# Performance work log

Measured on AMD Instinct MI355X. Metric: run time of the kernel, lower is better.

## Reference

```python
import jax, jax.numpy as jnp
import numpy as np

NUM_HEADS = 8
NUM_GROUPS = 32
EMB = 512
EPS = 1e-5


def setup_inputs() -> dict:
    key = jax.random.key(0)
    ks = jax.random.split(key, 12)
    B, C, H, W = 256, EMB, 16, 16
    s = 1.0 / np.sqrt(C)
    x = jax.random.normal(ks[0], (B, C, H, W), dtype=jnp.float32)
    Wq = jax.random.normal(ks[1], (C, EMB), dtype=jnp.float32) * s
    bq = jax.random.normal(ks[2], (EMB,), dtype=jnp.float32) * 0.01
    Wk = jax.random.normal(ks[3], (C, EMB), dtype=jnp.float32) * s
    bk = jax.random.normal(ks[4], (EMB,), dtype=jnp.float32) * 0.01
    Wv = jax.random.normal(ks[5], (C, EMB), dtype=jnp.float32) * s
    bv = jax.random.normal(ks[6], (EMB,), dtype=jnp.float32) * 0.01
    Wf = jax.random.normal(ks[7], (EMB, EMB), dtype=jnp.float32) * s
    bf = jax.random.normal(ks[8], (EMB,), dtype=jnp.float32) * 0.01
    gn_w = jnp.ones((EMB,), dtype=jnp.float32)
    gn_b = jnp.zeros((EMB,), dtype=jnp.float32)
    return {"x": x, "Wq": Wq, "bq": bq, "Wk": Wk, "bk": bk,
            "Wv": Wv, "bv": bv, "Wf": Wf, "bf": bf,
            "gn_w": gn_w, "gn_b": gn_b}


def reference(x, Wq, bq, Wk, bk, Wv, bv, Wf, bf, gn_w, gn_b):
    B, C, H, W = x.shape
    S = H * W
    nh = NUM_HEADS
    dh = EMB // nh
    xs = x.reshape(B, C, S).transpose(0, 2, 1)  # [B, S, C]
    q = (xs @ Wq + bq).reshape(B, S, nh, dh)
    k = (xs @ Wk + bk).reshape(B, S, nh, dh)
    v = (xs @ Wv + bv).reshape(B, S, nh, dh)
    scale = dh ** -0.5
    logits = jnp.einsum('bshd,bthd->bhst', q, k) * scale  # [B, nh, S, S]
    attn = jax.nn.softmax(logits, axis=-1)
    o = jnp.einsum('bhst,bthd->bshd', attn, v).reshape(B, S, EMB)
    o = o @ Wf + bf  # [B, S, EMB]
    y = o.transpose(0, 2, 1).reshape(B, EMB, H, W) + x  # residual
    # GroupNorm over (channels-within-group, H, W)
    G = NUM_GROUPS
    yg = y.reshape(B, G, EMB // G, H, W)
    mu = jnp.mean(yg, axis=(2, 3, 4), keepdims=True)
    var = jnp.var(yg, axis=(2, 3, 4), keepdims=True)
    yn = ((yg - mu) * jax.lax.rsqrt(var + EPS)).reshape(B, EMB, H, W)
    return yn * gn_w.reshape(1, EMB, 1, 1) + gn_b.reshape(1, EMB, 1, 1)
```

## Files before the change

### kernel.cpp

```cpp
#include <hip/hip_runtime.h>
#include <hip/hip_bf16.h>
#include <stdint.h>

#define B_  256
#define C_  512
#define S_  256
#define NH  8
#define DH  64

typedef float f32x4 __attribute__((ext_vector_type(4)));
typedef short s16x8 __attribute__((ext_vector_type(8)));

static __device__ __forceinline__ unsigned short f2bf(float f) {
  union { float f; unsigned u; } v; v.f = f;
  unsigned r = v.u + 0x7FFFu + ((v.u >> 16) & 1u);
  return (unsigned short)(r >> 16);
}

static __device__ __forceinline__ unsigned pk_bf16(float lo, float hi) {
  unsigned r;
  asm("v_cvt_pk_bf16_f32 %0, %1, %2" : "=v"(r) : "v"(lo), "v"(hi));
  return r;
}

static __device__ __forceinline__ void gload_lds16(const void* g, void* l) {
  __builtin_amdgcn_global_load_lds((const __attribute__((address_space(1))) void*)g,
                                   (__attribute__((address_space(3))) void*)l,
                                   16, 0, 0);
}

__global__ __launch_bounds__(256) void prep(const float* __restrict__ x,
                                            const float* __restrict__ Wq,
                                            const float* __restrict__ Wk,
                                            const float* __restrict__ Wv,
                                            const float* __restrict__ Wf,
                                            unsigned short* __restrict__ Whead,
                                            unsigned short* __restrict__ Wft,
                                            unsigned short* __restrict__ xs) {
  __shared__ float tile[64][65];
  int bid = blockIdx.x;
  int t = threadIdx.x;
  int tr = t >> 4;
  int tc = (t & 15) * 4;
  if (bid < 8192) {
    int b = bid >> 5, rem = bid & 31;
    int s0 = (rem & 3) * 64, c0 = (rem >> 2) * 64;
    const float* xb = x + (size_t)b * C_ * S_;
#pragma unroll
    for (int i = 0; i < 4; ++i) {
      int c = tr + i * 16;
      float4 v = *(const float4*)&xb[(size_t)(c0 + c) * S_ + s0 + tc];
      tile[c][tc + 0] = v.x; tile[c][tc + 1] = v.y;
      tile[c][tc + 2] = v.z; tile[c][tc + 3] = v.w;
    }
    __syncthreads();
    unsigned short* xsb = xs + (size_t)b * S_ * C_;
#pragma unroll
    for (int i = 0; i < 4; ++i) {
      int s = tr + i * 16;
      ushort4 o;
      o.x = f2bf(tile[tc + 0][s]); o.y = f2bf(tile[tc + 1][s]);
      o.z = f2bf(tile[tc + 2][s]); o.w = f2bf(tile[tc + 3][s]);
      *(ushort4*)&xsb[(size_t)(s0 + s) * C_ + c0 + tc] = o;
    }
  } else {
    int r = bid - 8192;
    int mat = r >> 6, r6 = r & 63;
    int n0 = (r6 & 7) * 64, c0 = (r6 >> 3) * 64;
    const float* src = (mat == 0) ? Wq : (mat == 1) ? Wk : (mat == 2) ? Wv : Wf;
#pragma unroll
    for (int i = 0; i < 4; ++i) {
      int c = tr + i * 16;
      float4 v = *(const float4*)&src[(size_t)(c0 + c) * 512 + n0 + tc];
      tile[c][tc + 0] = v.x; tile[c][tc + 1] = v.y;
      tile[c][tc + 2] = v.z; tile[c][tc + 3] = v.w;
    }
    __syncthreads();
    int h = n0 >> 6;
    unsigned short* dst = (mat < 3) ? (Whead + ((size_t)h * 192 + mat * 64) * 512)
                                    : (Wft + (size_t)n0 * 512);
#pragma unroll
    for (int i = 0; i < 4; ++i) {
      int nl = tr + i * 16;
      ushort4 o;
      o.x = f2bf(tile[tc + 0][nl]); o.y = f2bf(tile[tc + 1][nl]);
      o.z = f2bf(tile[tc + 2][nl]); o.w = f2bf(tile[tc + 3][nl]);
      *(ushort4*)&dst[(size_t)nl * 512 + c0 + tc] = o;
    }
  }
}

#define QKP 68
#define QOFF 0
#define KOFF 34816
#define VOFF 69632
__global__ __launch_bounds__(512) void qkvattn(const unsigned short* __restrict__ xs,
                                               const unsigned short* __restrict__ Whead,
                                               const float* __restrict__ bq,
                                               const float* __restrict__ bk,
                                               const float* __restrict__ bv,
                                               unsigned short* __restrict__ o) {
  __shared__ __align__(16) char lds[114688];
  int bid = blockIdx.x;
  int lin = (bid & 7) * 256 + (bid >> 3);
  int h = lin & 7, b = lin >> 3;
  int t = threadIdx.x, lane = t & 63, w = t >> 6;
  int l15 = lane & 15, l4 = lane >> 4;
  int wr = w >> 2, wc = w & 3;
  const unsigned short* xsb = xs + (size_t)b * S_ * C_;
  const unsigned short* wh  = Whead + (size_t)h * 192 * C_;

#define FSTAGE(kt, p)                                                         \
  {                                                                           \
    _Pragma("unroll")                                                         \
    for (int i = 0; i < 4; ++i) {                                             \
      int ch = i * 512 + t, r = ch >> 3, g = ch & 7;                          \
      int gs = g ^ (r & 7);                                                   \
      gload_lds16(xsb + (size_t)r * C_ + (kt) * 64 + gs * 8,                  \
                  lds + (p) * 57344 + ch * 16);                               \
    }                                                                         \
    _Pragma("unroll")                                                         \
    for (int i = 0; i < 3; ++i) {                                             \
      int ch = i * 512 + t, r = ch >> 3, g = ch & 7;                          \
      int gs = g ^ (r & 7);                                                   \
      gload_lds16(wh + (size_t)r * C_ + (kt) * 64 + gs * 8,                   \
                  lds + (p) * 57344 + 32768 + ch * 16);                       \
    }                                                                         \
  }

  f32x4 acc[8][3] = {};
  FSTAGE(0, 0);

  for (int kt = 0; kt < 8; ++kt) {
    if (kt < 7) FSTAGE(kt + 1, (kt + 1) & 1);
    if (kt < 7) asm volatile("s_waitcnt vmcnt(7)" ::: "memory");
    else        asm volatile("s_waitcnt vmcnt(0)" ::: "memory");
    __builtin_amdgcn_s_barrier();
    asm volatile("" ::: "memory");
    const char* Ab = lds + (kt & 1) * 57344;
    const char* Bb = Ab + 32768;
#pragma unroll
    for (int kk = 0; kk < 2; ++kk) {
      s16x8 afr[8], bfr[3];
#pragma unroll
      for (int fi = 0; fi < 8; ++fi) {
        int r = wr * 128 + fi * 16 + l15;
        afr[fi] = *(const s16x8*)(Ab + r * 128 + (((kk * 4 + l4) ^ (r & 7)) << 4));
      }
#pragma unroll
      for (int fj = 0; fj < 3; ++fj) {
        int r = wc * 48 + fj * 16 + l15;
        bfr[fj] = *(const s16x8*)(Bb + r * 128 + (((kk * 4 + l4) ^ (r & 7)) << 4));
      }
      __builtin_amdgcn_s_setprio(1);
#pragma unroll
      for (int fi = 0; fi < 8; ++fi)
#pragma unroll
        for (int fj = 0; fj < 3; ++fj)
          acc[fi][fj] = __builtin_amdgcn_mfma_f32_16x16x32_bf16(afr[fi], bfr[fj], acc[fi][fj], 0, 0, 0);
      __builtin_amdgcn_s_setprio(0);
    }
    __builtin_amdgcn_s_barrier();
  }
#undef FSTAGE

  unsigned short* Ql = (unsigned short*)(lds + QOFF);
  unsigned short* Kl = (unsigned short*)(lds + KOFF);
  unsigned short* Vl = (unsigned short*)(lds + VOFF);
  int h64 = h * 64;
#pragma unroll
  for (int fj = 0; fj < 3; ++fj) {
    int n = wc * 48 + fj * 16 + l15;
    int sel = n >> 6, d = n & 63;
    const float* bias = (sel == 0) ? bq : (sel == 1) ? bk : bv;
    float bias_v = bias[h64 + d];
    if (sel == 2) {
#pragma unroll
      for (int fi = 0; fi < 8; ++fi) {
        int s0 = wr * 128 + fi * 16 + l4 * 4;
        ushort4 o4;
        o4.x = f2bf(acc[fi][fj][0] + bias_v);
        o4.y = f2bf(acc[fi][fj][1] + bias_v);
        o4.z = f2bf(acc[fi][fj][2] + bias_v);
        o4.w = f2bf(acc[fi][fj][3] + bias_v);
        *(ushort4*)&Vl[d * 264 + s0] = o4;
      }
    } else {
      unsigned short* dstl = (sel == 0) ? Ql : Kl;
#pragma unroll
      for (int fi = 0; fi < 8; ++fi)
#pragma unroll
        for (int rg = 0; rg < 4; ++rg) {
          int s = wr * 128 + fi * 16 + l4 * 4 + rg;
          int row = s;
          if (sel == 1) {
            int s64 = s & 63, w32 = s64 & 31;
            row = (s & 192) + (s64 >> 5) * 32 + ((w32 >> 2) & 1) * 16 + (w32 >> 3) * 4 + (w32 & 3);
          }
          dstl[row * QKP + d] = f2bf(acc[fi][fj][rg] + bias_v);
        }
    }
  }
  __syncthreads();

  s16x8 qf[2][2];
#pragma unroll
  for (int fi = 0; fi < 2; ++fi)
#pragma unroll
    for (int kk = 0; kk < 2; ++kk) {
      int row = w * 32 + fi * 16 + l15;
      qf[fi][kk] = *(const s16x8*)((const char*)lds + QOFF + row * (QKP * 2) + kk * 64 + l4 * 16);
    }

  f32x4 acco[4][2] = {};
  float m_run[2] = {-3e38f, -3e38f}, l_run[2] = {0.f, 0.f};
  const float SCL = 0.125f * 1.44269504089f;

  for (int kb = 0; kb < 4; ++kb) {
    f32x4 accs[4][2] = {};
#pragma unroll
    for (int kk = 0; kk < 2; ++kk) {
      s16x8 kf[4];
#pragma unroll
      for (int fj = 0; fj < 4; ++fj)
        kf[fj] = *(const s16x8*)((const char*)lds + KOFF + (kb * 64 + fj * 16 + l15) * (QKP * 2) + kk * 64 + l4 * 16);
      __builtin_amdgcn_s_setprio(1);
#pragma unroll
      for (int fj = 0; fj < 4; ++fj)
#pragma unroll
        for (int fi = 0; fi < 2; ++fi)
          accs[fj][fi] = __builtin_amdgcn_mfma_f32_16x16x32_bf16(kf[fj], qf[fi][kk], accs[fj][fi], 0, 0, 0);
      __builtin_amdgcn_s_setprio(0);
    }
#pragma unroll
    for (int fi = 0; fi < 2; ++fi) {
      float m0[4];
#pragma unroll
      for (int fj = 0; fj < 4; ++fj)
        m0[fj] = fmaxf(fmaxf(accs[fj][fi][0], accs[fj][fi][1]),
                       fmaxf(accs[fj][fi][2], accs[fj][fi][3]));
      float mx = fmaxf(fmaxf(m0[0], m0[1]), fmaxf(m0[2], m0[3]));
      mx = fmaxf(mx, __shfl_xor(mx, 16, 64));
      mx = fmaxf(mx, __shfl_xor(mx, 32, 64));
      float mnew = fmaxf(m_run[fi], mx);
      float alpha = __builtin_amdgcn_exp2f((m_run[fi] - mnew) * SCL);
      m_run[fi] = mnew;
      float s0[4];
#pragma unroll
      for (int fj = 0; fj < 4; ++fj) {
#pragma unroll
        for (int rg = 0; rg < 4; ++rg) {
          float p = __builtin_amdgcn_exp2f((accs[fj][fi][rg] - mnew) * SCL);
          accs[fj][fi][rg] = p;
        }
        s0[fj] = (accs[fj][fi][0] + accs[fj][fi][1]) + (accs[fj][fi][2] + accs[fj][fi][3]);
      }
      float lsum = (s0[0] + s0[1]) + (s0[2] + s0[3]);
      lsum += __shfl_xor(lsum, 16, 64);
      lsum += __shfl_xor(lsum, 32, 64);
      l_run[fi] = l_run[fi] * alpha + lsum;
#pragma unroll
      for (int fd = 0; fd < 4; ++fd)
#pragma unroll
        for (int rg = 0; rg < 4; ++rg) acco[fd][fi][rg] *= alpha;
    }
#pragma unroll
    for (int kk2 = 0; kk2 < 2; ++kk2) {
      s16x8 vf[4];
#pragma unroll
      for (int fd = 0; fd < 4; ++fd)
        vf[fd] = *(const s16x8*)((const char*)lds + VOFF + (fd * 16 + l15) * 528 + kb * 128 + kk2 * 64 + l4 * 16);
#pragma unroll
      for (int fi = 0; fi < 2; ++fi) {
        union { unsigned u[4]; s16x8 v; } pb;
        pb.u[0] = pk_bf16(accs[2 * kk2][fi][0],     accs[2 * kk2][fi][1]);
        pb.u[1] = pk_bf16(accs[2 * kk2][fi][2],     accs[2 * kk2][fi][3]);
        pb.u[2] = pk_bf16(accs[2 * kk2 + 1][fi][0], accs[2 * kk2 + 1][fi][1]);
        pb.u[3] = pk_bf16(accs[2 * kk2 + 1][fi][2], accs[2 * kk2 + 1][fi][3]);
        __builtin_amdgcn_s_setprio(1);
#pragma unroll
        for (int fd = 0; fd < 4; ++fd)
          acco[fd][fi] = __builtin_amdgcn_mfma_f32_16x16x32_bf16(vf[fd], pb.v, acco[fd][fi], 0, 0, 0);
        __builtin_amdgcn_s_setprio(0);
      }
    }
  }

  unsigned short* ob = o + (size_t)b * S_ * C_ + h * DH;
#pragma unroll
  for (int fi = 0; fi < 2; ++fi) {
    float inv = 1.0f / l_run[fi];
    int qrow = w * 32 + fi * 16 + l15;
#pragma unroll
    for (int fd = 0; fd < 4; ++fd) {
      ushort4 s4;
      s4.x = f2bf(acco[fd][fi][0] * inv);
      s4.y = f2bf(acco[fd][fi][1] * inv);
      s4.z = f2bf(acco[fd][fi][2] * inv);
      s4.w = f2bf(acco[fd][fi][3] * inv);
      *(ushort4*)&ob[(size_t)qrow * C_ + fd * 16 + l4 * 4] = s4;
    }
  }
}

__global__ __launch_bounds__(512, 4) void proj_gn(const unsigned short* __restrict__ o,
                                                  const unsigned short* __restrict__ Wft,
                                                  const float* __restrict__ bfp,
                                                  const float* __restrict__ x,
                                                  const float* __restrict__ gnw,
                                                  const float* __restrict__ gnb,
                                                  float* __restrict__ out) {
  __shared__ __align__(16) char plds[40960];
  __shared__ float red_s[64], red_q[64];
  __shared__ float mu_s[4], rs_s[4];
  int bid = blockIdx.x;
  int lin = (bid & 7) * 256 + (bid >> 3);
  int b = lin >> 3, ct = lin & 7;
  int t = threadIdx.x, lane = t & 63, w = t >> 6;
  int l15 = lane & 15, l4 = lane >> 4;
  if (t < 64) { red_s[t] = 0.f; red_q[t] = 0.f; }
  f32x4 acc[4][2] = {};
  const unsigned short* wt = Wft + (size_t)ct * 64 * C_;
  const unsigned short* ob = o + (size_t)b * S_ * C_;

#define PSTAGE(kt, p)                                                         \
  {                                                                           \
    if (t < 256) {                                                            \
      int r = t >> 2, g = t & 3;                                              \
      int gs = g ^ ((r >> 1) & 3);                                            \
      gload_lds16(wt + (size_t)r * C_ + (kt) * 32 + gs * 8,                   \
                  plds + (p) * 20480 + t * 16);                               \
    }                                                                         \
    _Pragma("unroll")                                                         \
    for (int i = 0; i < 2; ++i) {                                             \
      int ch = i * 512 + t, r = ch >> 2, g = ch & 3;                          \
      int gs = g ^ ((r >> 1) & 3);                                            \
      gload_lds16(ob + (size_t)r * C_ + (kt) * 32 + gs * 8,                   \
                  plds + (p) * 20480 + 4096 + ch * 16);                       \
    }                                                                         \
  }

  PSTAGE(0, 0);

  for (int kt = 0; kt < 16; ++kt) {
    if (kt < 15) {
      PSTAGE(kt + 1, (kt + 1) & 1);
      if (t < 256) asm volatile("s_waitcnt vmcnt(3)" ::: "memory");
      else         asm volatile("s_waitcnt vmcnt(2)" ::: "memory");
    } else {
      asm volatile("s_waitcnt vmcnt(0)" ::: "memory");
    }
    __builtin_amdgcn_s_barrier();
    asm volatile("" ::: "memory");
    const char* Ab = plds + (kt & 1) * 20480;
    const char* Bb = Ab + 4096;
    s16x8 af[4], bfr[2];
#pragma unroll
    for (int fi = 0; fi < 4; ++fi) {
      int r = fi * 16 + l15;
      af[fi] = *(const s16x8*)(Ab + r * 64 + ((l4 ^ ((r >> 1) & 3)) << 4));
    }
#pragma unroll
    for (int fj = 0; fj < 2; ++fj) {
      int r = w * 32 + fj * 16 + l15;
      bfr[fj] = *(const s16x8*)(Bb + r * 64 + ((l4 ^ ((r >> 1) & 3)) << 4));
    }
    __builtin_amdgcn_s_setprio(1);
#pragma unroll
    for (int fi = 0; fi < 4; ++fi)
#pragma unroll
      for (int fj = 0; fj < 2; ++fj)
        acc[fi][fj] = __builtin_amdgcn_mfma_f32_16x16x32_bf16(af[fi], bfr[fj], acc[fi][fj], 0, 0, 0);
    __builtin_amdgcn_s_setprio(0);
    __builtin_amdgcn_s_barrier();
  }
#undef PSTAGE

  const float* xb = x + (size_t)b * C_ * S_;
  int c_base = ct * 64;
  int s_base = w * 32;
#pragma unroll
  for (int fi = 0; fi < 4; ++fi)
#pragma unroll
    for (int rg = 0; rg < 4; ++rg) {
      int cl = fi * 16 + l4 * 4 + rg;
      int c = c_base + cl;
      float bias_v = bfp[c];
      float psum = 0.f, psq = 0.f;
#pragma unroll
      for (int fj = 0; fj < 2; ++fj) {
        int s = s_base + fj * 16 + l15;
        float y = acc[fi][fj][rg] + bias_v + xb[(size_t)c * S_ + s];
        acc[fi][fj][rg] = y;
        psum += y; psq += y * y;
      }
#pragma unroll
      for (int off = 1; off < 16; off <<= 1) {
        psum += __shfl_xor(psum, off, 64);
        psq += __shfl_xor(psq, off, 64);
      }
      if (l15 == 0) {
        atomicAdd(&red_s[cl], psum);
        atomicAdd(&red_q[cl], psq);
      }
    }
  __syncthreads();
  if (t < 4) {
    float s = 0.f, qq = 0.f;
#pragma unroll
    for (int i = 0; i < 16; ++i) { s += red_s[t * 16 + i]; qq += red_q[t * 16 + i]; }
    float mu = s * (1.0f / 4096.0f);
    float var = qq * (1.0f / 4096.0f) - mu * mu;
    mu_s[t] = mu;
    rs_s[t] = rsqrtf(var + 1e-5f);
  }
  __syncthreads();
  float* outb = out + (size_t)b * C_ * S_;
#pragma unroll
  for (int fi = 0; fi < 4; ++fi)
#pragma unroll
    for (int rg = 0; rg < 4; ++rg) {
      int cl = fi * 16 + l4 * 4 + rg;
      int c = c_base + cl;
      int gl = cl >> 4;
      float mu = mu_s[gl], rs = rs_s[gl];
      float gw = gnw[c], gb = gnb[c];
#pragma unroll
      for (int fj = 0; fj < 2; ++fj) {
        int s = s_base + fj * 16 + l15;
        outb[(size_t)c * S_ + s] = (acc[fi][fj][rg] - mu) * rs * gw + gb;
      }
    }
}

extern "C" void kernel_launch(void* const* d_in, const int* in_sizes, int n_in,
                              void* d_out, int out_size, void* d_ws, size_t ws_size,
                              hipStream_t stream) {
  const float* x   = (const float*)d_in[0];
  const float* Wq  = (const float*)d_in[1];
  const float* bq  = (const float*)d_in[2];
  const float* Wk  = (const float*)d_in[3];
  const float* bk  = (const float*)d_in[4];
  const float* Wv  = (const float*)d_in[5];
  const float* bv  = (const float*)d_in[6];
  const float* Wf  = (const float*)d_in[7];
  const float* bf  = (const float*)d_in[8];
  const float* gnw = (const float*)d_in[9];
  const float* gnb = (const float*)d_in[10];

  char* ws = (char*)d_ws;
  unsigned short* Whead = (unsigned short*)ws;
  unsigned short* Wft   = (unsigned short*)(ws + 0x180000);
  unsigned short* xs    = (unsigned short*)(ws + 0x200000);
  unsigned short* obuf  = (unsigned short*)(ws + 0x200000 + (size_t)B_ * S_ * C_ * 2);
  float* out = (float*)d_out;

  hipLaunchKernelGGL(prep, dim3(8448), dim3(256), 0, stream,
                     x, Wq, Wk, Wv, Wf, Whead, Wft, xs);
  hipLaunchKernelGGL(qkvattn, dim3(2048), dim3(512), 0, stream,
                     xs, Whead, bq, bk, bv, obuf);
  hipLaunchKernelGGL(proj_gn, dim3(2048), dim3(512), 0, stream,
                     obuf, Wft, bf, x, gnw, gnb, out);
}
```

Baseline: 314.7 us.

## Transpose QKV projection MFMA tiling to vectorize Q/K LDS stores

Swaps the operand roles in the fused QKV projection so weight rows feed the A slot and x rows feed the B slot. The per-wave tile changes from 8x3 to 6x4 fragments, which puts four consecutive head dims in each lane. This lets the Q/K epilogue pack two bf16 pairs into one 8-byte LDS store and load the bias as a float4. V is now written with scalar stores and a new row stride of 266 elements to reduce bank conflicts. That stride leaves the 16-byte V fragment reads in the attention loop misaligned, which may split into narrower loads or be unsafe.

```diff
diff --git a/kernel.cpp b/kernel.cpp
--- a/kernel.cpp
+++ b/kernel.cpp
@@ -94,6 +94,7 @@
 #define QOFF 0
 #define KOFF 34816
 #define VOFF 69632
+#define VSTR 266
 __global__ __launch_bounds__(512) void qkvattn(const unsigned short* __restrict__ xs,
                                                const unsigned short* __restrict__ Whead,
                                                const float* __restrict__ bq,
@@ -128,7 +129,7 @@
     }                                                                         \
   }
 
-  f32x4 acc[8][3] = {};
+  f32x4 acc[6][4] = {};
   FSTAGE(0, 0);
 
   for (int kt = 0; kt < 8; ++kt) {
@@ -141,23 +142,23 @@
     const char* Bb = Ab + 32768;
 #pragma unroll
     for (int kk = 0; kk < 2; ++kk) {
-      s16x8 afr[8], bfr[3];
-#pragma unroll
-      for (int fi = 0; fi < 8; ++fi) {
-        int r = wr * 128 + fi * 16 + l15;
-        afr[fi] = *(const s16x8*)(Ab + r * 128 + (((kk * 4 + l4) ^ (r & 7)) << 4));
-      }
-#pragma unroll
-      for (int fj = 0; fj < 3; ++fj) {
-        int r = wc * 48 + fj * 16 + l15;
-        bfr[fj] = *(const s16x8*)(Bb + r * 128 + (((kk * 4 + l4) ^ (r & 7)) << 4));
+      s16x8 wfr[6], xfr[4];
+#pragma unroll
+      for (int fi = 0; fi < 6; ++fi) {
+        int r = wr * 96 + fi * 16 + l15;
+        wfr[fi] = *(const s16x8*)(Bb + r * 128 + (((kk * 4 + l4) ^ (r & 7)) << 4));
+      }
+#pragma unroll
+      for (int fj = 0; fj < 4; ++fj) {
+        int r = wc * 64 + fj * 16 + l15;
+        xfr[fj] = *(const s16x8*)(Ab + r * 128 + (((kk * 4 + l4) ^ (r & 7)) << 4));
       }
       __builtin_amdgcn_s_setprio(1);
 #pragma unroll
-      for (int fi = 0; fi < 8; ++fi)
-#pragma unroll
-        for (int fj = 0; fj < 3; ++fj)
-          acc[fi][fj] = __builtin_amdgcn_mfma_f32_16x16x32_bf16(afr[fi], bfr[fj], acc[fi][fj], 0, 0, 0);
+      for (int fi = 0; fi < 6; ++fi)
+#pragma unroll
+        for (int fj = 0; fj < 4; ++fj)
+          acc[fi][fj] = __builtin_amdgcn_mfma_f32_16x16x32_bf16(wfr[fi], xfr[fj], acc[fi][fj], 0, 0, 0);
       __builtin_amdgcn_s_setprio(0);
     }
     __builtin_amdgcn_s_barrier();
@@ -169,36 +170,36 @@
   unsigned short* Vl = (unsigned short*)(lds + VOFF);
   int h64 = h * 64;
 #pragma unroll
-  for (int fj = 0; fj < 3; ++fj) {
-    int n = wc * 48 + fj * 16 + l15;
-    int sel = n >> 6, d = n & 63;
+  for (int fi = 0; fi < 6; ++fi) {
+    int n0q = wr * 96 + fi * 16 + l4 * 4;
+    int sel = n0q >> 6;
+    int d0 = n0q & 63;
     const float* bias = (sel == 0) ? bq : (sel == 1) ? bk : bv;
-    float bias_v = bias[h64 + d];
+    float4 b4 = *(const float4*)&bias[h64 + d0];
     if (sel == 2) {
 #pragma unroll
-      for (int fi = 0; fi < 8; ++fi) {
-        int s0 = wr * 128 + fi * 16 + l4 * 4;
-        ushort4 o4;
-        o4.x = f2bf(acc[fi][fj][0] + bias_v);
-        o4.y = f2bf(acc[fi][fj][1] + bias_v);
-        o4.z = f2bf(acc[fi][fj][2] + bias_v);
-        o4.w = f2bf(acc[fi][fj][3] + bias_v);
-        *(ushort4*)&Vl[d * 264 + s0] = o4;
+      for (int fj = 0; fj < 4; ++fj) {
+        int s = wc * 64 + fj * 16 + l15;
+        Vl[(d0 + 0) * VSTR + s] = f2bf(acc[fi][fj][0] + b4.x);
+        Vl[(d0 + 1) * VSTR + s] = f2bf(acc[fi][fj][1] + b4.y);
+        Vl[(d0 + 2) * VSTR + s] = f2bf(acc[fi][fj][2] + b4.z);
+        Vl[(d0 + 3) * VSTR + s] = f2bf(acc[fi][fj][3] + b4.w);
       }
     } else {
       unsigned short* dstl = (sel == 0) ? Ql : Kl;
 #pragma unroll
-      for (int fi = 0; fi < 8; ++fi)
-#pragma unroll
-        for (int rg = 0; rg < 4; ++rg) {
-          int s = wr * 128 + fi * 16 + l4 * 4 + rg;
-          int row = s;
-          if (sel == 1) {
-            int s64 = s & 63, w32 = s64 & 31;
-            row = (s & 192) + (s64 >> 5) * 32 + ((w32 >> 2) & 1) * 16 + (w32 >> 3) * 4 + (w32 & 3);
-          }
-          dstl[row * QKP + d] = f2bf(acc[fi][fj][rg] + bias_v);
+      for (int fj = 0; fj < 4; ++fj) {
+        int s = wc * 64 + fj * 16 + l15;
+        int row = s;
+        if (sel == 1) {
+          int s64 = s & 63, w32 = s64 & 31;
+          row = (s & 192) + (s64 >> 5) * 32 + ((w32 >> 2) & 1) * 16 + (w32 >> 3) * 4 + (w32 & 3);
         }
+        unsigned u0 = pk_bf16(acc[fi][fj][0] + b4.x, acc[fi][fj][1] + b4.y);
+        unsigned u1 = pk_bf16(acc[fi][fj][2] + b4.z, acc[fi][fj][3] + b4.w);
+        uint2 val; val.x = u0; val.y = u1;
+        *(uint2*)&dstl[row * QKP + d0] = val;
+      }
     }
   }
   __syncthreads();
@@ -269,7 +270,7 @@
       s16x8 vf[4];
 #pragma unroll
       for (int fd = 0; fd < 4; ++fd)
-        vf[fd] = *(const s16x8*)((const char*)lds + VOFF + (fd * 16 + l15) * 528 + kb * 128 + kk2 * 64 + l4 * 16);
+        vf[fd] = *(const s16x8*)((const char*)lds + VOFF + (fd * 16 + l15) * (VSTR * 2) + kb * 128 + kk2 * 64 + l4 * 16);
 #pragma unroll
       for (int fi = 0; fi < 2; ++fi) {
         union { unsigned u[4]; s16x8 v; } pb;
```

Result: no change. 315.0 us (+0.1%).

## Double qkvattn block to 1024 threads, halving per-wave tiles

Applied to the files above, without the earlier changes.

The fused QKV-projection and attention kernel now runs 16 waves per block instead of 8. Each wave owns a 64x48 projection tile and 16 query rows instead of 128x48 and 32 rows. The staging loads are redistributed over 1024 threads, with per-thread vmcnt waits adjusted to match. The aim is more latency hiding per CU with fewer accumulator registers per wave. The cost is less reuse of fragments loaded from LDS and more barrier participants, and LDS use (about 112KB per block) still limits the CU to one block.

```diff
diff --git a/kernel.cpp b/kernel.cpp
--- a/kernel.cpp
+++ b/kernel.cpp
@@ -94,12 +94,12 @@
 #define QOFF 0
 #define KOFF 34816
 #define VOFF 69632
-__global__ __launch_bounds__(512) void qkvattn(const unsigned short* __restrict__ xs,
-                                               const unsigned short* __restrict__ Whead,
-                                               const float* __restrict__ bq,
-                                               const float* __restrict__ bk,
-                                               const float* __restrict__ bv,
-                                               unsigned short* __restrict__ o) {
+__global__ __launch_bounds__(1024, 4) void qkvattn(const unsigned short* __restrict__ xs,
+                                                   const unsigned short* __restrict__ Whead,
+                                                   const float* __restrict__ bq,
+                                                   const float* __restrict__ bk,
+                                                   const float* __restrict__ bv,
+                                                   unsigned short* __restrict__ o) {
   __shared__ __align__(16) char lds[114688];
   int bid = blockIdx.x;
   int lin = (bid & 7) * 256 + (bid >> 3);
@@ -113,38 +113,47 @@
 #define FSTAGE(kt, p)                                                         \
   {                                                                           \
     _Pragma("unroll")                                                         \
-    for (int i = 0; i < 4; ++i) {                                             \
-      int ch = i * 512 + t, r = ch >> 3, g = ch & 7;                          \
+    for (int i = 0; i < 2; ++i) {                                             \
+      int ch = i * 1024 + t, r = ch >> 3, g = ch & 7;                         \
       int gs = g ^ (r & 7);                                                   \
       gload_lds16(xsb + (size_t)r * C_ + (kt) * 64 + gs * 8,                  \
                   lds + (p) * 57344 + ch * 16);                               \
     }                                                                         \
-    _Pragma("unroll")                                                         \
-    for (int i = 0; i < 3; ++i) {                                             \
-      int ch = i * 512 + t, r = ch >> 3, g = ch & 7;                          \
+    {                                                                         \
+      int ch = t, r = ch >> 3, g = ch & 7;                                    \
       int gs = g ^ (r & 7);                                                   \
       gload_lds16(wh + (size_t)r * C_ + (kt) * 64 + gs * 8,                   \
                   lds + (p) * 57344 + 32768 + ch * 16);                       \
     }                                                                         \
-  }
-
-  f32x4 acc[8][3] = {};
+    if (t < 512) {                                                            \
+      int ch = 1024 + t, r = ch >> 3, g = ch & 7;                             \
+      int gs = g ^ (r & 7);                                                   \
+      gload_lds16(wh + (size_t)r * C_ + (kt) * 64 + gs * 8,                   \
+                  lds + (p) * 57344 + 32768 + ch * 16);                       \
+    }                                                                         \
+  }
+
+  f32x4 acc[4][3] = {};
   FSTAGE(0, 0);
 
   for (int kt = 0; kt < 8; ++kt) {
-    if (kt < 7) FSTAGE(kt + 1, (kt + 1) & 1);
-    if (kt < 7) asm volatile("s_waitcnt vmcnt(7)" ::: "memory");
-    else        asm volatile("s_waitcnt vmcnt(0)" ::: "memory");
+    if (kt < 7) {
+      FSTAGE(kt + 1, (kt + 1) & 1);
+      if (t < 512) asm volatile("s_waitcnt vmcnt(4)" ::: "memory");
+      else         asm volatile("s_waitcnt vmcnt(3)" ::: "memory");
+    } else {
+      asm volatile("s_waitcnt vmcnt(0)" ::: "memory");
+    }
     __builtin_amdgcn_s_barrier();
     asm volatile("" ::: "memory");
     const char* Ab = lds + (kt & 1) * 57344;
     const char* Bb = Ab + 32768;
 #pragma unroll
     for (int kk = 0; kk < 2; ++kk) {
-      s16x8 afr[8], bfr[3];
-#pragma unroll
-      for (int fi = 0; fi < 8; ++fi) {
-        int r = wr * 128 + fi * 16 + l15;
+      s16x8 afr[4], bfr[3];
+#pragma unroll
+      for (int fi = 0; fi < 4; ++fi) {
+        int r = wr * 64 + fi * 16 + l15;
         afr[fi] = *(const s16x8*)(Ab + r * 128 + (((kk * 4 + l4) ^ (r & 7)) << 4));
       }
 #pragma unroll
@@ -154,7 +163,7 @@
       }
       __builtin_amdgcn_s_setprio(1);
 #pragma unroll
-      for (int fi = 0; fi < 8; ++fi)
+      for (int fi = 0; fi < 4; ++fi)
 #pragma unroll
         for (int fj = 0; fj < 3; ++fj)
           acc[fi][fj] = __builtin_amdgcn_mfma_f32_16x16x32_bf16(afr[fi], bfr[fj], acc[fi][fj], 0, 0, 0);
@@ -176,8 +185,8 @@
     float bias_v = bias[h64 + d];
     if (sel == 2) {
 #pragma unroll
-      for (int fi = 0; fi < 8; ++fi) {
-        int s0 = wr * 128 + fi * 16 + l4 * 4;
+      for (int fi = 0; fi < 4; ++fi) {
+        int s0 = wr * 64 + fi * 16 + l4 * 4;
         ushort4 o4;
         o4.x = f2bf(acc[fi][fj][0] + bias_v);
         o4.y = f2bf(acc[fi][fj][1] + bias_v);
@@ -188,10 +197,10 @@
     } else {
       unsigned short* dstl = (sel == 0) ? Ql : Kl;
 #pragma unroll
-      for (int fi = 0; fi < 8; ++fi)
+      for (int fi = 0; fi < 4; ++fi)
 #pragma unroll
         for (int rg = 0; rg < 4; ++rg) {
-          int s = wr * 128 + fi * 16 + l4 * 4 + rg;
+          int s = wr * 64 + fi * 16 + l4 * 4 + rg;
           int row = s;
           if (sel == 1) {
             int s64 = s & 63, w32 = s64 & 31;
@@ -203,21 +212,19 @@
   }
   __syncthreads();
 
-  s16x8 qf[2][2];
-#pragma unroll
-  for (int fi = 0; fi < 2; ++fi)
-#pragma unroll
-    for (int kk = 0; kk < 2; ++kk) {
-      int row = w * 32 + fi * 16 + l15;
-      qf[fi][kk] = *(const s16x8*)((const char*)lds + QOFF + row * (QKP * 2) + kk * 64 + l4 * 16);
-    }
-
-  f32x4 acco[4][2] = {};
-  float m_run[2] = {-3e38f, -3e38f}, l_run[2] = {0.f, 0.f};
+  s16x8 qf[2];
+#pragma unroll
+  for (int kk = 0; kk < 2; ++kk) {
+    int row = w * 16 + l15;
+    qf[kk] = *(const s16x8*)((const char*)lds + QOFF + row * (QKP * 2) + kk * 64 + l4 * 16);
+  }
+
+  f32x4 acco[4] = {};
+  float m_run = -3e38f, l_run = 0.f;
   const float SCL = 0.125f * 1.44269504089f;
 
   for (int kb = 0; kb < 4; ++kb) {
-    f32x4 accs[4][2] = {};
+    f32x4 accs[4] = {};
 #pragma unroll
     for (int kk = 0; kk < 2; ++kk) {
       s16x8 kf[4];
@@ -227,42 +234,38 @@
       __builtin_amdgcn_s_setprio(1);
 #pragma unroll
       for (int fj = 0; fj < 4; ++fj)
-#pragma unroll
-        for (int fi = 0; fi < 2; ++fi)
-          accs[fj][fi] = __builtin_amdgcn_mfma_f32_16x16x32_bf16(kf[fj], qf[fi][kk], accs[fj][fi], 0, 0, 0);
+        accs[fj] = __builtin_amdgcn_mfma_f32_16x16x32_bf16(kf[fj], qf[kk], accs[fj], 0, 0, 0);
       __builtin_amdgcn_s_setprio(0);
     }
-#pragma unroll
-    for (int fi = 0; fi < 2; ++fi) {
+    {
       float m0[4];
 #pragma unroll
       for (int fj = 0; fj < 4; ++fj)
-        m0[fj] = fmaxf(fmaxf(accs[fj][fi][0], accs[fj][fi][1]),
-                       fmaxf(accs[fj][fi][2], accs[fj][fi][3]));
+        m0[fj] = fmaxf(fmaxf(accs[fj][0], accs[fj][1]), fmaxf(accs[fj][2], accs[fj][3]));
       float mx = fmaxf(fmaxf(m0[0], m0[1]), fmaxf(m0[2], m0[3]));
       mx = fmaxf(mx, __shfl_xor(mx, 16, 64));
       mx = fmaxf(mx, __shfl_xor(mx, 32, 64));
-      float mnew = fmaxf(m_run[fi], mx);
-      float alpha = __builtin_amdgcn_exp2f((m_run[fi] - mnew) * SCL);
-      m_run[fi] = mnew;
+      float mnew = fmaxf(m_run, mx);
+      float alpha = __builtin_amdgcn_exp2f((m_run - mnew) * SCL);
+      m_run = mnew;
       float s0[4];
 #pragma unroll
       for (int fj = 0; fj < 4; ++fj) {
 #pragma unroll
         for (int rg = 0; rg < 4; ++rg) {
-          float p = __builtin_amdgcn_exp2f((accs[fj][fi][rg] - mnew) * SCL);
-          accs[fj][fi][rg] = p;
+          float p = __builtin_amdgcn_exp2f((accs[fj][rg] - mnew) * SCL);
+          accs[fj][rg] = p;
         }
-        s0[fj] = (accs[fj][fi][0] + accs[fj][fi][1]) + (accs[fj][fi][2] + accs[fj][fi][3]);
+        s0[fj] = (accs[fj][0] + accs[fj][1]) + (accs[fj][2] + accs[fj][3]);
       }
       float lsum = (s0[0] + s0[1]) + (s0[2] + s0[3]);
       lsum += __shfl_xor(lsum, 16, 64);
       lsum += __shfl_xor(lsum, 32, 64);
-      l_run[fi] = l_run[fi] * alpha + lsum;
+      l_run = l_run * alpha + lsum;
 #pragma unroll
       for (int fd = 0; fd < 4; ++fd)
 #pragma unroll
-        for (int rg = 0; rg < 4; ++rg) acco[fd][fi][rg] *= alpha;
+        for (int rg = 0; rg < 4; ++rg) acco[fd][rg] *= alpha;
     }
 #pragma unroll
     for (int kk2 = 0; kk2 < 2; ++kk2) {
@@ -270,34 +273,30 @@
 #pragma unroll
       for (int fd = 0; fd < 4; ++fd)
         vf[fd] = *(const s16x8*)((const char*)lds + VOFF + (fd * 16 + l15) * 528 + kb * 128 + kk2 * 64 + l4 * 16);
-#pragma unroll
-      for (int fi = 0; fi < 2; ++fi) {
-        union { unsigned u[4]; s16x8 v; } pb;
-        pb.u[0] = pk_bf16(accs[2 * kk2][fi][0],     accs[2 * kk2][fi][1]);
-        pb.u[1] = pk_bf16(accs[2 * kk2][fi][2],     accs[2 * kk2][fi][3]);
-        pb.u[2] = pk_bf16(accs[2 * kk2 + 1][fi][0], accs[2 * kk2 + 1][fi][1]);
-        pb.u[3] = pk_bf16(accs[2 * kk2 + 1][fi][2], accs[2 * kk2 + 1][fi][3]);
-        __builtin_amdgcn_s_setprio(1);
-#pragma unroll
-        for (int fd = 0; fd < 4; ++fd)
-          acco[fd][fi] = __builtin_amdgcn_mfma_f32_16x16x32_bf16(vf[fd], pb.v, acco[fd][fi], 0, 0, 0);
-        __builtin_amdgcn_s_setprio(0);
-      }
+      union { unsigned u[4]; s16x8 v; } pb;
+      pb.u[0] = pk_bf16(accs[2 * kk2][0],     accs[2 * kk2][1]);
+      pb.u[1] = pk_bf16(accs[2 * kk2][2],     accs[2 * kk2][3]);
+      pb.u[2] = pk_bf16(accs[2 * kk2 + 1][0], accs[2 * kk2 + 1][1]);
+      pb.u[3] = pk_bf16(accs[2 * kk2 + 1][2], accs[2 * kk2 + 1][3]);
+      __builtin_amdgcn_s_setprio(1);
+#pragma unroll
+      for (int fd = 0; fd < 4; ++fd)
+        acco[fd] = __builtin_amdgcn_mfma_f32_16x16x32_bf16(vf[fd], pb.v, acco[fd], 0, 0, 0);
+      __builtin_amdgcn_s_setprio(0);
     }
   }
 
   unsigned short* ob = o + (size_t)b * S_ * C_ + h * DH;
-#pragma unroll
-  for (int fi = 0; fi < 2; ++fi) {
-    float inv = 1.0f / l_run[fi];
-    int qrow = w * 32 + fi * 16 + l15;
+  {
+    float inv = 1.0f / l_run;
+    int qrow = w * 16 + l15;
 #pragma unroll
     for (int fd = 0; fd < 4; ++fd) {
       ushort4 s4;
-      s4.x = f2bf(acco[fd][fi][0] * inv);
-      s4.y = f2bf(acco[fd][fi][1] * inv);
-      s4.z = f2bf(acco[fd][fi][2] * inv);
-      s4.w = f2bf(acco[fd][fi][3] * inv);
+      s4.x = f2bf(acco[fd][0] * inv);
+      s4.y = f2bf(acco[fd][1] * inv);
+      s4.z = f2bf(acco[fd][2] * inv);
+      s4.w = f2bf(acco[fd][3] * inv);
       *(ushort4*)&ob[(size_t)qrow * C_ + fd * 16 + l4 * 4] = s4;
     }
   }
@@ -457,7 +456,7 @@
 
   hipLaunchKernelGGL(prep, dim3(8448), dim3(256), 0, stream,
                      x, Wq, Wk, Wv, Wf, Whead, Wft, xs);
-  hipLaunchKernelGGL(qkvattn, dim3(2048), dim3(512), 0, stream,
+  hipLaunchKernelGGL(qkvattn, dim3(2048), dim3(1024), 0, stream,
                      xs, Whead, bq, bk, bv, obuf);
   hipLaunchKernelGGL(proj_gn, dim3(2048), dim3(512), 0, stream,
                      obuf, Wft, bf, x, gnw, gnb, out);
```

Result: no change. 312.3 us (-0.8%).
